# Kernel tuning notes

Measured on AMD Instinct MI355X. Metric: run time of the kernel, lower is better.

## Reference

```python
import jax, jax.numpy as jnp
import numpy as np

N_NODES = 100000
N_EDGES = 3200000
N_FEAT = 256
HIDDEN = 64
N_CLASSES = 6


def gcn_conv(x, W, b, src, dst, n_nodes):
    """PyG GCNConv: out = D^{-1/2} (A + I) D^{-1/2} X W + b (self-loops added)."""
    h = x @ W  # [N, out]
    loops = jnp.arange(n_nodes, dtype=src.dtype)
    src2 = jnp.concatenate([src, loops])
    dst2 = jnp.concatenate([dst, loops])
    # degree over destination nodes (edge weight 1), including self-loops
    deg = jax.ops.segment_sum(jnp.ones_like(dst2, dtype=h.dtype), dst2,
                              num_segments=n_nodes)
    dis = jnp.where(deg > 0, jax.lax.rsqrt(deg), 0.0)  # deg^{-1/2}
    norm = dis[src2] * dis[dst2]  # [E+N]
    msg = h[src2] * norm[:, None]  # gather + scale
    out = jax.ops.segment_sum(msg, dst2, num_segments=n_nodes)  # scatter-add
    return out + b


def setup_inputs() -> dict:
    key = jax.random.key(0)
    ks = jax.random.split(key, 5)
    x = jax.random.normal(ks[0], (N_NODES, N_FEAT), dtype=jnp.float32)
    edge_index = jax.random.randint(ks[1], (2, N_EDGES), 0, N_NODES, dtype=jnp.int64)
    W1 = jax.random.normal(ks[2], (N_FEAT, HIDDEN), dtype=jnp.float32) / np.sqrt(N_FEAT)
    b1 = jnp.zeros((HIDDEN,), dtype=jnp.float32)
    W2 = jax.random.normal(ks[3], (HIDDEN, HIDDEN), dtype=jnp.float32) / np.sqrt(HIDDEN)
    b2 = jnp.zeros((HIDDEN,), dtype=jnp.float32)
    Wfc = jax.random.normal(ks[4], (HIDDEN, N_CLASSES), dtype=jnp.float32) / np.sqrt(HIDDEN)
    bfc = jnp.zeros((N_CLASSES,), dtype=jnp.float32)
    return {"x": x, "edge_index": edge_index, "W1": W1, "b1": b1,
            "W2": W2, "b2": b2, "Wfc": Wfc, "bfc": bfc}


def reference(x, edge_index, W1, b1, W2, b2, Wfc, bfc):
    src, dst = edge_index[0], edge_index[1]
    n = x.shape[0]
    h = jax.nn.relu(gcn_conv(x, W1, b1, src, dst, n))
    # dropout(p=0.2) is identity in eval mode
    h = jax.nn.relu(gcn_conv(h, W2, b2, src, dst, n))
    return h @ Wfc + bfc
```

## Files before the change

kernel.cpp:

```cpp
#include <hip/hip_runtime.h>
#include <hip/hip_fp16.h>
#include <math.h>

#define NFEAT 256
#define HID 64
#define NCLS 6
#define NBMX 1600
#define CAPB 4096
#define CHUNK 16384
#define FUSED_LDS 32768

typedef float vf4 __attribute__((ext_vector_type(4)));
typedef int   vi4 __attribute__((ext_vector_type(4)));


__global__ __launch_bounds__(256) void k_count(const int* __restrict__ dst,
                                               int* __restrict__ C, int E, int nbuck) {
  __shared__ int cnt[NBMX];
  int t = threadIdx.x;
  for (int i = t; i < nbuck; i += 256) cnt[i] = 0;
  __syncthreads();
  int e0 = blockIdx.x * CHUNK;
  int e1 = e0 + CHUNK;
  if (e1 > E) e1 = E;
  for (int r0 = e0; r0 < e1; r0 += 1024) {
    int i0 = r0 + t * 4;
    if (i0 + 4 <= e1) {
      vi4 dv = __builtin_nontemporal_load((const vi4*)&dst[i0]);
      atomicAdd(&cnt[dv.x >> 6], 1);
      atomicAdd(&cnt[dv.y >> 6], 1);
      atomicAdd(&cnt[dv.z >> 6], 1);
      atomicAdd(&cnt[dv.w >> 6], 1);
    } else {
      for (int q = 0; q < 4; ++q)
        if (i0 + q < e1) atomicAdd(&cnt[dst[i0 + q] >> 6], 1);
    }
  }
  __syncthreads();
  int* Crow = C + (size_t)blockIdx.x * nbuck;
  for (int i = t; i < nbuck; i += 256) Crow[i] = cnt[i];
}


__global__ __launch_bounds__(256) void k_scan_cols(int* __restrict__ C,
                                                   int* __restrict__ T,
                                                   int nblk, int nbuck) {
  int b = blockIdx.x * 256 + threadIdx.x;
  if (b >= nbuck) return;
  int run = 0;
  int blk = 0;
  for (; blk + 4 <= nblk; blk += 4) {
    int c0 = C[(size_t)(blk + 0) * nbuck + b];
    int c1 = C[(size_t)(blk + 1) * nbuck + b];
    int c2 = C[(size_t)(blk + 2) * nbuck + b];
    int c3 = C[(size_t)(blk + 3) * nbuck + b];
    C[(size_t)(blk + 0) * nbuck + b] = run; run += c0;
    C[(size_t)(blk + 1) * nbuck + b] = run; run += c1;
    C[(size_t)(blk + 2) * nbuck + b] = run; run += c2;
    C[(size_t)(blk + 3) * nbuck + b] = run; run += c3;
  }
  for (; blk < nblk; ++blk) {
    int c = C[(size_t)blk * nbuck + b];
    C[(size_t)blk * nbuck + b] = run;
    run += c;
  }
  T[b] = run;
}


__global__ __launch_bounds__(256) void k_scanb(const int* __restrict__ T,
                                               int* __restrict__ bbase, int nbuck) {
  __shared__ int sh[256];
  __shared__ int carry;
  int t = threadIdx.x;
  if (t == 0) carry = 0;
  __syncthreads();
  for (int base = 0; base < nbuck; base += 256) {
    int v = (base + t < nbuck) ? T[base + t] : 0;
    sh[t] = v;
    __syncthreads();
    for (int off = 1; off < 256; off <<= 1) {
      int x = sh[t];
      int y = (t >= off) ? sh[t - off] : 0;
      __syncthreads();
      sh[t] = x + y;
      __syncthreads();
    }
    if (base + t < nbuck) bbase[base + t] = carry + sh[t] - v;
    __syncthreads();
    if (t == 255) carry += sh[255];
    __syncthreads();
  }
}


__global__ __launch_bounds__(256) void k_fused(const int* __restrict__ src,
                                               const int* __restrict__ dst,
                                               const int* __restrict__ C,
                                               const int* __restrict__ bbase,
                                               unsigned* __restrict__ packed,
                                               int E, int nbuck, int nbb,
                                               const float* __restrict__ X,
                                               const float* __restrict__ W1,
                                               __half* __restrict__ H16, int n) {
  extern __shared__ char smem[];
  int t = threadIdx.x;

  if (blockIdx.x < nbb) {
    int* baseL = (int*)smem;
    int* cnt   = baseL + NBMX;
    const int* Crow = C + (size_t)blockIdx.x * nbuck;
    for (int i = t; i < nbuck; i += 256) {
      baseL[i] = bbase[i] + Crow[i];
      cnt[i] = 0;
    }
    __syncthreads();

    int e0 = blockIdx.x * CHUNK;
    int e1 = e0 + CHUNK;
    if (e1 > E) e1 = E;
    for (int r0 = e0; r0 < e1; r0 += 1024) {
      int i0 = r0 + t * 4;
      int s4[4], d4[4];
      bool full = (i0 + 4 <= e1);
      if (full) {
        vi4 sv = __builtin_nontemporal_load((const vi4*)&src[i0]);
        vi4 dv = __builtin_nontemporal_load((const vi4*)&dst[i0]);
        s4[0] = sv.x; s4[1] = sv.y; s4[2] = sv.z; s4[3] = sv.w;
        d4[0] = dv.x; d4[1] = dv.y; d4[2] = dv.z; d4[3] = dv.w;
      } else {
        for (int q = 0; q < 4; ++q)
          if (i0 + q < e1) { s4[q] = src[i0 + q]; d4[q] = dst[i0 + q]; }
      }
#pragma unroll
      for (int q = 0; q < 4; ++q) {
        if (i0 + q < e1) {
          int b = d4[q] >> 6;
          int slot = atomicAdd(&cnt[b], 1);
          packed[(size_t)baseL[b] + slot] =
              ((unsigned)s4[q] << 6) | (unsigned)(d4[q] & 63);
        }
      }
    }
  } else {
    float* Wl = (float*)smem;
    float* Xl = Wl + 4096;
    const int row0 = (blockIdx.x - nbb) * 64;
    const int tc = t & 15;
    const int tr = t >> 4;
    float acc[4][4] = {};

    for (int k0 = 0; k0 < NFEAT; k0 += 64) {
      __syncthreads();
#pragma unroll
      for (int i = 0; i < 4; ++i) {
        int idx = t * 4 + i * 1024;
        int kr = idx >> 6, c = idx & 63;
        *(vf4*)&Wl[idx] = *(const vf4*)&W1[(size_t)(k0 + kr) * 64 + c];
      }
#pragma unroll
      for (int i = 0; i < 4; ++i) {
        int idx = t * 4 + i * 1024;
        int r = idx >> 6, c = idx & 63;
        int row = row0 + r;
        vf4 v = {0.f, 0.f, 0.f, 0.f};
        if (row < n) v = __builtin_nontemporal_load((const vf4*)&X[(size_t)row * NFEAT + k0 + c]);
        *(vf4*)&Xl[idx] = v;
      }
      __syncthreads();
#pragma unroll 4
      for (int kk = 0; kk < 64; kk += 4) {
        float4 xv[4], wv[4];
#pragma unroll
        for (int r = 0; r < 4; ++r) xv[r] = *(float4*)&Xl[(tr * 4 + r) * 64 + kk];
#pragma unroll
        for (int q = 0; q < 4; ++q) wv[q] = *(float4*)&Wl[(kk + q) * 64 + tc * 4];
#pragma unroll
        for (int r = 0; r < 4; ++r) {
          const float xr[4] = {xv[r].x, xv[r].y, xv[r].z, xv[r].w};
#pragma unroll
          for (int q = 0; q < 4; ++q) {
            acc[r][0] += xr[q] * wv[q].x;
            acc[r][1] += xr[q] * wv[q].y;
            acc[r][2] += xr[q] * wv[q].z;
            acc[r][3] += xr[q] * wv[q].w;
          }
        }
      }
    }
#pragma unroll
    for (int r = 0; r < 4; ++r) {
      int row = row0 + tr * 4 + r;
      if (row < n) {
        __half2 h01 = __floats2half2_rn(acc[r][0], acc[r][1]);
        __half2 h23 = __floats2half2_rn(acc[r][2], acc[r][3]);
        uint2 st;
        st.x = *reinterpret_cast<unsigned*>(&h01);
        st.y = *reinterpret_cast<unsigned*>(&h23);
        ((uint2*)H16)[(size_t)row * 16 + tc] = st;
      }
    }
  }
}


__global__ __launch_bounds__(256) void k_build(unsigned* __restrict__ packed,
                                               const int* __restrict__ T,
                                               const int* __restrict__ bbase,
                                               int2* __restrict__ rowrange,
                                               float* __restrict__ dis,
                                               int n, int nbuck) {
  __shared__ unsigned buf[CAPB];
  __shared__ unsigned outb[CAPB];
  __shared__ int cnt4[4][64];
  __shared__ int cur4[4][64];
  __shared__ int offi[64];
  __shared__ int offx[64];
  __shared__ int cntl[64];
  int b = blockIdx.x;
  int t = threadIdx.x;
  int g = t >> 6;
  int m = T[b];
  if (m > CAPB) m = CAPB;
  int bb = bbase[b];
  unsigned* pb = packed + bb;

  cnt4[g][t & 63] = 0;
  for (int k = t; k < m; k += 256) buf[k] = pb[k];
  __syncthreads();
  for (int k = t; k < m; k += 256) atomicAdd(&cnt4[g][buf[k] & 63u], 1);
  __syncthreads();
  if (t < 64) {
    int c0 = cnt4[0][t], c1 = cnt4[1][t], c2 = cnt4[2][t], c3 = cnt4[3][t];
    int tot = c0 + c1 + c2 + c3;
    cntl[t] = tot;
    offi[t] = tot;
    cur4[0][t] = 0;
    cur4[1][t] = c0;
    cur4[2][t] = c0 + c1;
    cur4[3][t] = c0 + c1 + c2;
  }
  __syncthreads();
  for (int off = 1; off < 64; off <<= 1) {
    int x = (t < 64) ? offi[t] : 0;
    int y = (t >= off && t < 64) ? offi[t - off] : 0;
    __syncthreads();
    if (t < 64) offi[t] = x + y;
    __syncthreads();
  }
  if (t < 64) {
    offx[t] = offi[t] - cntl[t];
    int v = b * 64 + t;
    if (v < n) {
      rowrange[v] = make_int2(bb + offx[t], cntl[t]);
      dis[v] = rsqrtf((float)cntl[t] + 1.0f);
    }
#pragma unroll
    for (int gg = 0; gg < 4; ++gg) cur4[gg][t] += offx[t];
  }
  __syncthreads();
  for (int k = t; k < m; k += 256) {
    unsigned e = buf[k];
    int dl = e & 63u;
    int q = atomicAdd(&cur4[g][dl], 1);
    outb[q] = e >> 6;
  }
  __syncthreads();
  for (int k = t; k < m; k += 256) pb[k] = outb[k];
}


__global__ __launch_bounds__(256) void k_agg_w(const int2* __restrict__ rowrange,
                                               const int* __restrict__ srcs,
                                               const __half* __restrict__ g16,
                                               const float* __restrict__ dis,
                                               const float* __restrict__ bias,
                                               float* __restrict__ outp, int n) {
  int v = blockIdx.x * 16 + (threadIdx.x >> 4);
  if (v >= n) return;
  int lane = threadIdx.x & 15;
  int2 rr = rowrange[v];
  int j = rr.x, end = rr.x + rr.y;
  const uint2* g2 = (const uint2*)g16;

  float dv = dis[v];
  uint2 su = g2[(size_t)v * 16 + lane];
  float2 f0 = __half22float2(*reinterpret_cast<__half2*>(&su.x));
  float2 f1 = __half22float2(*reinterpret_cast<__half2*>(&su.y));
  float ax = dv * f0.x, ay = dv * f0.y, az = dv * f1.x, aw = dv * f1.y;

  for (; j + 8 <= end; j += 8) {
    int s[8];
#pragma unroll
    for (int q = 0; q < 8; ++q) s[q] = __builtin_nontemporal_load(&srcs[j + q]);
    float ds[8];
    uint2 a[8];
#pragma unroll
    for (int q = 0; q < 8; ++q) { ds[q] = dis[s[q]]; a[q] = g2[(size_t)s[q] * 16 + lane]; }
#pragma unroll
    for (int q = 0; q < 8; ++q) {
      float2 p0 = __half22float2(*reinterpret_cast<__half2*>(&a[q].x));
      float2 p1 = __half22float2(*reinterpret_cast<__half2*>(&a[q].y));
      ax = fmaf(ds[q], p0.x, ax); ay = fmaf(ds[q], p0.y, ay);
      az = fmaf(ds[q], p1.x, az); aw = fmaf(ds[q], p1.y, aw);
    }
  }
  for (; j < end; ++j) {
    int s0 = __builtin_nontemporal_load(&srcs[j]);
    float ds = dis[s0];
    uint2 a0 = g2[(size_t)s0 * 16 + lane];
    float2 p0 = __half22float2(*reinterpret_cast<__half2*>(&a0.x));
    float2 p1 = __half22float2(*reinterpret_cast<__half2*>(&a0.y));
    ax = fmaf(ds, p0.x, ax); ay = fmaf(ds, p0.y, ay);
    az = fmaf(ds, p1.x, az); aw = fmaf(ds, p1.y, aw);
  }

  float4 bb = *(const float4*)&bias[lane * 4];
  float4 o;
  o.x = fmaxf(fmaf(dv, ax, bb.x), 0.f);
  o.y = fmaxf(fmaf(dv, ay, bb.y), 0.f);
  o.z = fmaxf(fmaf(dv, az, bb.z), 0.f);
  o.w = fmaxf(fmaf(dv, aw, bb.w), 0.f);
  ((float4*)outp)[(size_t)v * 16 + lane] = o;
}


template<int K>
__global__ __launch_bounds__(256) void k_gemm_scaled(const float* __restrict__ X,
                                                     const float* __restrict__ W,
                                                     const float* __restrict__ dis,
                                                     __half* __restrict__ G16, int n) {
  __shared__ float Wl[64 * 64];
  __shared__ float Xl[64 * 64];
  const int tid = threadIdx.x;
  const int row0 = blockIdx.x * 64;
  const int tc = tid & 15;
  const int tr = tid >> 4;
  float acc[4][4] = {};

  for (int k0 = 0; k0 < K; k0 += 64) {
    __syncthreads();
#pragma unroll
    for (int i = 0; i < 4; ++i) {
      int idx = tid * 4 + i * 1024;
      int kr = idx >> 6, c = idx & 63;
      *(vf4*)&Wl[idx] = *(const vf4*)&W[(size_t)(k0 + kr) * 64 + c];
    }
#pragma unroll
    for (int i = 0; i < 4; ++i) {
      int idx = tid * 4 + i * 1024;
      int r = idx >> 6, c = idx & 63;
      int row = row0 + r;
      vf4 v = {0.f, 0.f, 0.f, 0.f};
      if (row < n) v = __builtin_nontemporal_load((const vf4*)&X[(size_t)row * K + k0 + c]);
      *(vf4*)&Xl[idx] = v;
    }
    __syncthreads();
#pragma unroll 4
    for (int kk = 0; kk < 64; kk += 4) {
      float4 xv[4], wv[4];
#pragma unroll
      for (int r = 0; r < 4; ++r) xv[r] = *(float4*)&Xl[(tr * 4 + r) * 64 + kk];
#pragma unroll
      for (int q = 0; q < 4; ++q) wv[q] = *(float4*)&Wl[(kk + q) * 64 + tc * 4];
#pragma unroll
      for (int r = 0; r < 4; ++r) {
        const float xr[4] = {xv[r].x, xv[r].y, xv[r].z, xv[r].w};
#pragma unroll
        for (int q = 0; q < 4; ++q) {
          acc[r][0] += xr[q] * wv[q].x;
          acc[r][1] += xr[q] * wv[q].y;
          acc[r][2] += xr[q] * wv[q].z;
          acc[r][3] += xr[q] * wv[q].w;
        }
      }
    }
  }
#pragma unroll
  for (int r = 0; r < 4; ++r) {
    int row = row0 + tr * 4 + r;
    if (row < n) {
      float s = dis[row];
      __half2 h01 = __floats2half2_rn(acc[r][0] * s, acc[r][1] * s);
      __half2 h23 = __floats2half2_rn(acc[r][2] * s, acc[r][3] * s);
      uint2 st;
      st.x = *reinterpret_cast<unsigned*>(&h01);
      st.y = *reinterpret_cast<unsigned*>(&h23);
      ((uint2*)G16)[(size_t)row * 16 + tc] = st;
    }
  }
}


__global__ __launch_bounds__(256) void k_agg_csr(const int2* __restrict__ rowrange,
                                                 const int* __restrict__ srcs,
                                                 const __half* __restrict__ g16,
                                                 const float* __restrict__ dis,
                                                 const float* __restrict__ bias,
                                                 float* __restrict__ outp, int n) {
  int v = blockIdx.x * 16 + (threadIdx.x >> 4);
  if (v >= n) return;
  int lane = threadIdx.x & 15;
  int2 rr = rowrange[v];
  int j = rr.x, end = rr.x + rr.y;
  const uint2* g2 = (const uint2*)g16;

  uint2 su = g2[(size_t)v * 16 + lane];
  float2 f0 = __half22float2(*reinterpret_cast<__half2*>(&su.x));
  float2 f1 = __half22float2(*reinterpret_cast<__half2*>(&su.y));
  float ax = f0.x, ay = f0.y, az = f1.x, aw = f1.y;

  for (; j + 8 <= end; j += 8) {
    int s[8];
#pragma unroll
    for (int q = 0; q < 8; ++q) s[q] = __builtin_nontemporal_load(&srcs[j + q]);
    uint2 a[8];
#pragma unroll
    for (int q = 0; q < 8; ++q) a[q] = g2[(size_t)s[q] * 16 + lane];
#pragma unroll
    for (int q = 0; q < 8; ++q) {
      float2 p0 = __half22float2(*reinterpret_cast<__half2*>(&a[q].x));
      float2 p1 = __half22float2(*reinterpret_cast<__half2*>(&a[q].y));
      ax += p0.x; ay += p0.y; az += p1.x; aw += p1.y;
    }
  }
  for (; j < end; ++j) {
    int s0 = __builtin_nontemporal_load(&srcs[j]);
    uint2 a0 = g2[(size_t)s0 * 16 + lane];
    float2 p0 = __half22float2(*reinterpret_cast<__half2*>(&a0.x));
    float2 p1 = __half22float2(*reinterpret_cast<__half2*>(&a0.y));
    ax += p0.x; ay += p0.y; az += p1.x; aw += p1.y;
  }

  float dv = dis[v];
  float4 bb = *(const float4*)&bias[lane * 4];
  float4 o;
  o.x = fmaxf(fmaf(dv, ax, bb.x), 0.f);
  o.y = fmaxf(fmaf(dv, ay, bb.y), 0.f);
  o.z = fmaxf(fmaf(dv, az, bb.z), 0.f);
  o.w = fmaxf(fmaf(dv, aw, bb.w), 0.f);
  ((float4*)outp)[(size_t)v * 16 + lane] = o;
}


__global__ __launch_bounds__(256) void k_fc(const float* __restrict__ A,
                                            const float* __restrict__ Wfc,
                                            const float* __restrict__ bfc,
                                            float* __restrict__ outp, int n) {
  __shared__ float Wl[64 * NCLS];
  __shared__ float bl[8];
  int tid = threadIdx.x;
  for (int i = tid; i < 64 * NCLS; i += 256) Wl[i] = Wfc[i];
  if (tid < NCLS) bl[tid] = bfc[tid];
  __syncthreads();
  int row = blockIdx.x * 256 + tid;
  if (row >= n) return;
  float accv[NCLS];
#pragma unroll
  for (int j = 0; j < NCLS; ++j) accv[j] = bl[j];
  const vf4* a4 = (const vf4*)&A[(size_t)row * 64];
#pragma unroll
  for (int k4 = 0; k4 < 16; ++k4) {
    vf4 a = __builtin_nontemporal_load(&a4[k4]);
    const float av[4] = {a.x, a.y, a.z, a.w};
#pragma unroll
    for (int q = 0; q < 4; ++q)
#pragma unroll
      for (int j = 0; j < NCLS; ++j) accv[j] += av[q] * Wl[(k4 * 4 + q) * NCLS + j];
  }
#pragma unroll
  for (int j = 0; j < NCLS; ++j) outp[(size_t)row * NCLS + j] = accv[j];
}


extern "C" void kernel_launch(void* const* d_in, const int* in_sizes, int n_in,
                              void* d_out, int out_size, void* d_ws, size_t ws_size,
                              hipStream_t stream) {
  const float* x   = (const float*)d_in[0];
  const int*   ei  = (const int*)d_in[1];
  const float* W1  = (const float*)d_in[2];
  const float* b1  = (const float*)d_in[3];
  const float* W2  = (const float*)d_in[4];
  const float* b2  = (const float*)d_in[5];
  const float* Wfc = (const float*)d_in[6];
  const float* bfc = (const float*)d_in[7];
  float* out = (float*)d_out;

  const int n = in_sizes[0] / NFEAT;
  const int E = in_sizes[1] / 2;
  const int* src = ei;
  const int* dst = ei + E;
  const int nbuck = (n + 63) >> 6;
  const int nbb = (E + CHUNK - 1) / CHUNK;
  const int ntile = (n + 63) / 64;

  char* ws = (char*)d_ws;
  size_t off = 0;
  auto alloc = [&](size_t bytes) -> void* {
    void* p = (void*)(ws + off);
    off += (bytes + 255) & ~(size_t)255;
    return p;
  };
  float* dis      = (float*)alloc((size_t)n * 4);
  int2*  rowrange = (int2*)alloc((size_t)n * 8);
  int*   C        = (int*)alloc((size_t)nbb * nbuck * 4);
  int*   T        = (int*)alloc((size_t)nbuck * 4);
  int*   bbase    = (int*)alloc((size_t)nbuck * 4);
  unsigned* packed = (unsigned*)alloc((size_t)E * 4);
  __half* bufA16  = (__half*)alloc((size_t)n * HID * 2);
  float* bufB     = (float*)alloc((size_t)n * HID * 4);

  k_count<<<nbb, 256, 0, stream>>>(dst, C, E, nbuck);
  k_scan_cols<<<(nbuck + 255) / 256, 256, 0, stream>>>(C, T, nbb, nbuck);
  k_scanb<<<1, 256, 0, stream>>>(T, bbase, nbuck);
  k_fused<<<nbb + ntile, 256, FUSED_LDS, stream>>>(src, dst, C, bbase, packed,
                                                   E, nbuck, nbb, x, W1, bufA16, n);
  k_build<<<nbuck, 256, 0, stream>>>(packed, T, bbase, rowrange, dis, n, nbuck);

  k_agg_w<<<(n + 15) / 16, 256, 0, stream>>>(rowrange, (const int*)packed, bufA16, dis, b1, bufB, n);

  k_gemm_scaled<HID><<<(n + 63) / 64, 256, 0, stream>>>(bufB, W2, dis, bufA16, n);
  k_agg_csr<<<(n + 15) / 16, 256, 0, stream>>>(rowrange, (const int*)packed, bufA16, dis, b2, bufB, n);

  k_fc<<<(n + 255) / 256, 256, 0, stream>>>(bufB, Wfc, bfc, out, n);
}
```

Before: 317.4 us.

## Fuse layer-1 aggregation with W2 GEMM and layer-2 aggregation with FC head

```diff
diff --git a/kernel.cpp b/kernel.cpp
--- a/kernel.cpp
+++ b/kernel.cpp
@@ -270,206 +270,171 @@
 }
 
 
-__global__ __launch_bounds__(256) void k_agg_w(const int2* __restrict__ rowrange,
-                                               const int* __restrict__ srcs,
-                                               const __half* __restrict__ g16,
-                                               const float* __restrict__ dis,
-                                               const float* __restrict__ bias,
-                                               float* __restrict__ outp, int n) {
-  int v = blockIdx.x * 16 + (threadIdx.x >> 4);
-  if (v >= n) return;
-  int lane = threadIdx.x & 15;
-  int2 rr = rowrange[v];
-  int j = rr.x, end = rr.x + rr.y;
+__global__ __launch_bounds__(256) void k_agg_gemm(const int2* __restrict__ rowrange,
+                                                  const int* __restrict__ srcs,
+                                                  const __half* __restrict__ g16,
+                                                  const float* __restrict__ dis,
+                                                  const float* __restrict__ b1,
+                                                  const float* __restrict__ W2,
+                                                  __half* __restrict__ g2out, int n) {
+  __shared__ float W2l[64 * 64];
+  __shared__ float arow[16][68];
+  int t = threadIdx.x;
+  for (int i = t * 4; i < 4096; i += 1024)
+    *(vf4*)&W2l[i] = *(const vf4*)&W2[i];
+
+  int grp = t >> 4, lane = t & 15;
+  int v = blockIdx.x * 16 + grp;
+  bool active = (v < n);
   const uint2* g2 = (const uint2*)g16;
 
-  float dv = dis[v];
-  uint2 su = g2[(size_t)v * 16 + lane];
-  float2 f0 = __half22float2(*reinterpret_cast<__half2*>(&su.x));
-  float2 f1 = __half22float2(*reinterpret_cast<__half2*>(&su.y));
-  float ax = dv * f0.x, ay = dv * f0.y, az = dv * f1.x, aw = dv * f1.y;
-
-  for (; j + 8 <= end; j += 8) {
-    int s[8];
-#pragma unroll
-    for (int q = 0; q < 8; ++q) s[q] = __builtin_nontemporal_load(&srcs[j + q]);
-    float ds[8];
-    uint2 a[8];
-#pragma unroll
-    for (int q = 0; q < 8; ++q) { ds[q] = dis[s[q]]; a[q] = g2[(size_t)s[q] * 16 + lane]; }
-#pragma unroll
-    for (int q = 0; q < 8; ++q) {
-      float2 p0 = __half22float2(*reinterpret_cast<__half2*>(&a[q].x));
-      float2 p1 = __half22float2(*reinterpret_cast<__half2*>(&a[q].y));
-      ax = fmaf(ds[q], p0.x, ax); ay = fmaf(ds[q], p0.y, ay);
-      az = fmaf(ds[q], p1.x, az); aw = fmaf(ds[q], p1.y, aw);
-    }
-  }
-  for (; j < end; ++j) {
-    int s0 = __builtin_nontemporal_load(&srcs[j]);
-    float ds = dis[s0];
-    uint2 a0 = g2[(size_t)s0 * 16 + lane];
-    float2 p0 = __half22float2(*reinterpret_cast<__half2*>(&a0.x));
-    float2 p1 = __half22float2(*reinterpret_cast<__half2*>(&a0.y));
-    ax = fmaf(ds, p0.x, ax); ay = fmaf(ds, p0.y, ay);
-    az = fmaf(ds, p1.x, az); aw = fmaf(ds, p1.y, aw);
-  }
-
-  float4 bb = *(const float4*)&bias[lane * 4];
-  float4 o;
-  o.x = fmaxf(fmaf(dv, ax, bb.x), 0.f);
-  o.y = fmaxf(fmaf(dv, ay, bb.y), 0.f);
-  o.z = fmaxf(fmaf(dv, az, bb.z), 0.f);
-  o.w = fmaxf(fmaf(dv, aw, bb.w), 0.f);
-  ((float4*)outp)[(size_t)v * 16 + lane] = o;
-}
-
-
-template<int K>
-__global__ __launch_bounds__(256) void k_gemm_scaled(const float* __restrict__ X,
-                                                     const float* __restrict__ W,
-                                                     const float* __restrict__ dis,
-                                                     __half* __restrict__ G16, int n) {
-  __shared__ float Wl[64 * 64];
-  __shared__ float Xl[64 * 64];
-  const int tid = threadIdx.x;
-  const int row0 = blockIdx.x * 64;
-  const int tc = tid & 15;
-  const int tr = tid >> 4;
-  float acc[4][4] = {};
-
-  for (int k0 = 0; k0 < K; k0 += 64) {
-    __syncthreads();
-#pragma unroll
-    for (int i = 0; i < 4; ++i) {
-      int idx = tid * 4 + i * 1024;
-      int kr = idx >> 6, c = idx & 63;
-      *(vf4*)&Wl[idx] = *(const vf4*)&W[(size_t)(k0 + kr) * 64 + c];
-    }
-#pragma unroll
-    for (int i = 0; i < 4; ++i) {
-      int idx = tid * 4 + i * 1024;
-      int r = idx >> 6, c = idx & 63;
-      int row = row0 + r;
-      vf4 v = {0.f, 0.f, 0.f, 0.f};
-      if (row < n) v = __builtin_nontemporal_load((const vf4*)&X[(size_t)row * K + k0 + c]);
-      *(vf4*)&Xl[idx] = v;
-    }
-    __syncthreads();
+  float rx = 0.f, ry = 0.f, rz = 0.f, rw = 0.f;
+  if (active) {
+    int2 rr = rowrange[v];
+    int j = rr.x, end = rr.x + rr.y;
+    float dv = dis[v];
+    uint2 su = g2[(size_t)v * 16 + lane];
+    float2 f0 = __half22float2(*reinterpret_cast<__half2*>(&su.x));
+    float2 f1 = __half22float2(*reinterpret_cast<__half2*>(&su.y));
+    float ax = dv * f0.x, ay = dv * f0.y, az = dv * f1.x, aw = dv * f1.y;
+
+    for (; j + 8 <= end; j += 8) {
+      int s[8];
+#pragma unroll
+      for (int q = 0; q < 8; ++q) s[q] = __builtin_nontemporal_load(&srcs[j + q]);
+      float ds[8];
+      uint2 a[8];
+#pragma unroll
+      for (int q = 0; q < 8; ++q) { ds[q] = dis[s[q]]; a[q] = g2[(size_t)s[q] * 16 + lane]; }
+#pragma unroll
+      for (int q = 0; q < 8; ++q) {
+        float2 p0 = __half22float2(*reinterpret_cast<__half2*>(&a[q].x));
+        float2 p1 = __half22float2(*reinterpret_cast<__half2*>(&a[q].y));
+        ax = fmaf(ds[q], p0.x, ax); ay = fmaf(ds[q], p0.y, ay);
+        az = fmaf(ds[q], p1.x, az); aw = fmaf(ds[q], p1.y, aw);
+      }
+    }
+    for (; j < end; ++j) {
+      int s0 = __builtin_nontemporal_load(&srcs[j]);
+      float ds = dis[s0];
+      uint2 a0 = g2[(size_t)s0 * 16 + lane];
+      float2 p0 = __half22float2(*reinterpret_cast<__half2*>(&a0.x));
+      float2 p1 = __half22float2(*reinterpret_cast<__half2*>(&a0.y));
+      ax = fmaf(ds, p0.x, ax); ay = fmaf(ds, p0.y, ay);
+      az = fmaf(ds, p1.x, az); aw = fmaf(ds, p1.y, aw);
+    }
+    float4 bb = *(const float4*)&b1[lane * 4];
+    rx = fmaxf(fmaf(dv, ax, bb.x), 0.f);
+    ry = fmaxf(fmaf(dv, ay, bb.y), 0.f);
+    rz = fmaxf(fmaf(dv, az, bb.z), 0.f);
+    rw = fmaxf(fmaf(dv, aw, bb.w), 0.f);
+  }
+  arow[grp][lane * 4 + 0] = rx;
+  arow[grp][lane * 4 + 1] = ry;
+  arow[grp][lane * 4 + 2] = rz;
+  arow[grp][lane * 4 + 3] = rw;
+  __syncthreads();
+
+  if (active) {
+    float o0 = 0.f, o1 = 0.f, o2 = 0.f, o3 = 0.f;
+    int c = lane * 4;
 #pragma unroll 4
-    for (int kk = 0; kk < 64; kk += 4) {
-      float4 xv[4], wv[4];
-#pragma unroll
-      for (int r = 0; r < 4; ++r) xv[r] = *(float4*)&Xl[(tr * 4 + r) * 64 + kk];
-#pragma unroll
-      for (int q = 0; q < 4; ++q) wv[q] = *(float4*)&Wl[(kk + q) * 64 + tc * 4];
-#pragma unroll
-      for (int r = 0; r < 4; ++r) {
-        const float xr[4] = {xv[r].x, xv[r].y, xv[r].z, xv[r].w};
-#pragma unroll
-        for (int q = 0; q < 4; ++q) {
-          acc[r][0] += xr[q] * wv[q].x;
-          acc[r][1] += xr[q] * wv[q].y;
-          acc[r][2] += xr[q] * wv[q].z;
-          acc[r][3] += xr[q] * wv[q].w;
-        }
-      }
-    }
-  }
-#pragma unroll
-  for (int r = 0; r < 4; ++r) {
-    int row = row0 + tr * 4 + r;
-    if (row < n) {
-      float s = dis[row];
-      __half2 h01 = __floats2half2_rn(acc[r][0] * s, acc[r][1] * s);
-      __half2 h23 = __floats2half2_rn(acc[r][2] * s, acc[r][3] * s);
-      uint2 st;
-      st.x = *reinterpret_cast<unsigned*>(&h01);
-      st.y = *reinterpret_cast<unsigned*>(&h23);
-      ((uint2*)G16)[(size_t)row * 16 + tc] = st;
-    }
-  }
-}
-
-
-__global__ __launch_bounds__(256) void k_agg_csr(const int2* __restrict__ rowrange,
-                                                 const int* __restrict__ srcs,
-                                                 const __half* __restrict__ g16,
-                                                 const float* __restrict__ dis,
-                                                 const float* __restrict__ bias,
-                                                 float* __restrict__ outp, int n) {
-  int v = blockIdx.x * 16 + (threadIdx.x >> 4);
-  if (v >= n) return;
-  int lane = threadIdx.x & 15;
-  int2 rr = rowrange[v];
-  int j = rr.x, end = rr.x + rr.y;
-  const uint2* g2 = (const uint2*)g16;
-
-  uint2 su = g2[(size_t)v * 16 + lane];
-  float2 f0 = __half22float2(*reinterpret_cast<__half2*>(&su.x));
-  float2 f1 = __half22float2(*reinterpret_cast<__half2*>(&su.y));
-  float ax = f0.x, ay = f0.y, az = f1.x, aw = f1.y;
-
-  for (; j + 8 <= end; j += 8) {
-    int s[8];
-#pragma unroll
-    for (int q = 0; q < 8; ++q) s[q] = __builtin_nontemporal_load(&srcs[j + q]);
-    uint2 a[8];
-#pragma unroll
-    for (int q = 0; q < 8; ++q) a[q] = g2[(size_t)s[q] * 16 + lane];
-#pragma unroll
-    for (int q = 0; q < 8; ++q) {
-      float2 p0 = __half22float2(*reinterpret_cast<__half2*>(&a[q].x));
-      float2 p1 = __half22float2(*reinterpret_cast<__half2*>(&a[q].y));
-      ax += p0.x; ay += p0.y; az += p1.x; aw += p1.y;
-    }
-  }
-  for (; j < end; ++j) {
-    int s0 = __builtin_nontemporal_load(&srcs[j]);
-    uint2 a0 = g2[(size_t)s0 * 16 + lane];
-    float2 p0 = __half22float2(*reinterpret_cast<__half2*>(&a0.x));
-    float2 p1 = __half22float2(*reinterpret_cast<__half2*>(&a0.y));
-    ax += p0.x; ay += p0.y; az += p1.x; aw += p1.y;
-  }
-
-  float dv = dis[v];
-  float4 bb = *(const float4*)&bias[lane * 4];
-  float4 o;
-  o.x = fmaxf(fmaf(dv, ax, bb.x), 0.f);
-  o.y = fmaxf(fmaf(dv, ay, bb.y), 0.f);
-  o.z = fmaxf(fmaf(dv, az, bb.z), 0.f);
-  o.w = fmaxf(fmaf(dv, aw, bb.w), 0.f);
-  ((float4*)outp)[(size_t)v * 16 + lane] = o;
-}
-
-
-__global__ __launch_bounds__(256) void k_fc(const float* __restrict__ A,
-                                            const float* __restrict__ Wfc,
-                                            const float* __restrict__ bfc,
-                                            float* __restrict__ outp, int n) {
+    for (int k = 0; k < 64; ++k) {
+      float a = arow[grp][k];
+      vf4 w = *(const vf4*)&W2l[k * 64 + c];
+      o0 = fmaf(a, w.x, o0);
+      o1 = fmaf(a, w.y, o1);
+      o2 = fmaf(a, w.z, o2);
+      o3 = fmaf(a, w.w, o3);
+    }
+    float dvv = dis[v];
+    __half2 h01 = __floats2half2_rn(o0 * dvv, o1 * dvv);
+    __half2 h23 = __floats2half2_rn(o2 * dvv, o3 * dvv);
+    uint2 st;
+    st.x = *reinterpret_cast<unsigned*>(&h01);
+    st.y = *reinterpret_cast<unsigned*>(&h23);
+    ((uint2*)g2out)[(size_t)v * 16 + lane] = st;
+  }
+}
+
+
+__global__ __launch_bounds__(256) void k_agg_fc(const int2* __restrict__ rowrange,
+                                                const int* __restrict__ srcs,
+                                                const __half* __restrict__ g16,
+                                                const float* __restrict__ dis,
+                                                const float* __restrict__ b2,
+                                                const float* __restrict__ Wfc,
+                                                const float* __restrict__ bfc,
+                                                float* __restrict__ outp, int n) {
   __shared__ float Wl[64 * NCLS];
   __shared__ float bl[8];
-  int tid = threadIdx.x;
-  for (int i = tid; i < 64 * NCLS; i += 256) Wl[i] = Wfc[i];
-  if (tid < NCLS) bl[tid] = bfc[tid];
-  __syncthreads();
-  int row = blockIdx.x * 256 + tid;
-  if (row >= n) return;
-  float accv[NCLS];
-#pragma unroll
-  for (int j = 0; j < NCLS; ++j) accv[j] = bl[j];
-  const vf4* a4 = (const vf4*)&A[(size_t)row * 64];
-#pragma unroll
-  for (int k4 = 0; k4 < 16; ++k4) {
-    vf4 a = __builtin_nontemporal_load(&a4[k4]);
-    const float av[4] = {a.x, a.y, a.z, a.w};
-#pragma unroll
-    for (int q = 0; q < 4; ++q)
-#pragma unroll
-      for (int j = 0; j < NCLS; ++j) accv[j] += av[q] * Wl[(k4 * 4 + q) * NCLS + j];
-  }
-#pragma unroll
-  for (int j = 0; j < NCLS; ++j) outp[(size_t)row * NCLS + j] = accv[j];
+  int t = threadIdx.x;
+  for (int i = t; i < 64 * NCLS; i += 256) Wl[i] = Wfc[i];
+  if (t < NCLS) bl[t] = bfc[t];
+  __syncthreads();
+
+  int grp = t >> 4, lane = t & 15;
+  int v = blockIdx.x * 16 + grp;
+  bool active = (v < n);
+  const uint2* g2 = (const uint2*)g16;
+
+  float r0 = 0.f, r1 = 0.f, r2 = 0.f, r3 = 0.f;
+  if (active) {
+    int2 rr = rowrange[v];
+    int j = rr.x, end = rr.x + rr.y;
+    uint2 su = g2[(size_t)v * 16 + lane];
+    float2 f0 = __half22float2(*reinterpret_cast<__half2*>(&su.x));
+    float2 f1 = __half22float2(*reinterpret_cast<__half2*>(&su.y));
+    float ax = f0.x, ay = f0.y, az = f1.x, aw = f1.y;
+
+    for (; j + 8 <= end; j += 8) {
+      int s[8];
+#pragma unroll
+      for (int q = 0; q < 8; ++q) s[q] = __builtin_nontemporal_load(&srcs[j + q]);
+      uint2 a[8];
+#pragma unroll
+      for (int q = 0; q < 8; ++q) a[q] = g2[(size_t)s[q] * 16 + lane];
+#pragma unroll
+      for (int q = 0; q < 8; ++q) {
+        float2 p0 = __half22float2(*reinterpret_cast<__half2*>(&a[q].x));
+        float2 p1 = __half22float2(*reinterpret_cast<__half2*>(&a[q].y));
+        ax += p0.x; ay += p0.y; az += p1.x; aw += p1.y;
+      }
+    }
+    for (; j < end; ++j) {
+      int s0 = __builtin_nontemporal_load(&srcs[j]);
+      uint2 a0 = g2[(size_t)s0 * 16 + lane];
+      float2 p0 = __half22float2(*reinterpret_cast<__half2*>(&a0.x));
+      float2 p1 = __half22float2(*reinterpret_cast<__half2*>(&a0.y));
+      ax += p0.x; ay += p0.y; az += p1.x; aw += p1.y;
+    }
+    float dv = dis[v];
+    float4 bb = *(const float4*)&b2[lane * 4];
+    r0 = fmaxf(fmaf(dv, ax, bb.x), 0.f);
+    r1 = fmaxf(fmaf(dv, ay, bb.y), 0.f);
+    r2 = fmaxf(fmaf(dv, az, bb.z), 0.f);
+    r3 = fmaxf(fmaf(dv, aw, bb.w), 0.f);
+  }
+
+  float p[NCLS];
+#pragma unroll
+  for (int jj = 0; jj < NCLS; ++jj) p[jj] = 0.f;
+  int k0 = lane * 4;
+#pragma unroll
+  for (int q = 0; q < 4; ++q) {
+    float a = (q == 0) ? r0 : (q == 1) ? r1 : (q == 2) ? r2 : r3;
+#pragma unroll
+    for (int jj = 0; jj < NCLS; ++jj)
+      p[jj] = fmaf(a, Wl[(k0 + q) * NCLS + jj], p[jj]);
+  }
+#pragma unroll
+  for (int m = 1; m < 16; m <<= 1) {
+#pragma unroll
+    for (int jj = 0; jj < NCLS; ++jj)
+      p[jj] += __shfl_xor(p[jj], m, 64);
+  }
+  if (active && lane < NCLS)
+    outp[(size_t)v * NCLS + lane] = p[lane] + bl[lane];
 }
 
 
@@ -508,7 +473,7 @@
   int*   bbase    = (int*)alloc((size_t)nbuck * 4);
   unsigned* packed = (unsigned*)alloc((size_t)E * 4);
   __half* bufA16  = (__half*)alloc((size_t)n * HID * 2);
-  float* bufB     = (float*)alloc((size_t)n * HID * 4);
+  __half* bufC16  = (__half*)alloc((size_t)n * HID * 2);
 
   k_count<<<nbb, 256, 0, stream>>>(dst, C, E, nbuck);
   k_scan_cols<<<(nbuck + 255) / 256, 256, 0, stream>>>(C, T, nbb, nbuck);
@@ -517,10 +482,9 @@
                                                    E, nbuck, nbb, x, W1, bufA16, n);
   k_build<<<nbuck, 256, 0, stream>>>(packed, T, bbase, rowrange, dis, n, nbuck);
 
-  k_agg_w<<<(n + 15) / 16, 256, 0, stream>>>(rowrange, (const int*)packed, bufA16, dis, b1, bufB, n);
-
-  k_gemm_scaled<HID><<<(n + 63) / 64, 256, 0, stream>>>(bufB, W2, dis, bufA16, n);
-  k_agg_csr<<<(n + 15) / 16, 256, 0, stream>>>(rowrange, (const int*)packed, bufA16, dis, b2, bufB, n);
-
-  k_fc<<<(n + 255) / 256, 256, 0, stream>>>(bufB, Wfc, bfc, out, n);
-}
+  k_agg_gemm<<<(n + 15) / 16, 256, 0, stream>>>(rowrange, (const int*)packed, bufA16,
+                                                dis, b1, W2, bufC16, n);
+
+  k_agg_fc<<<(n + 15) / 16, 256, 0, stream>>>(rowrange, (const int*)packed, bufC16,
+                                              dis, b2, Wfc, bfc, out, n);
+}
```

Result: faster. 286.2 us (-9.8%).
